# Kernel optimization log

Hardware: AMD Instinct MI355X
Metric: run time of the kernel (lower is better)

Reference implementation:

```python
import jax, jax.numpy as jnp
import numpy as np

MODES = 256


def setup_inputs() -> dict:
    key = jax.random.key(0)
    k1, k2, k3, k4, k5 = jax.random.split(key, 5)
    B, C_IN, C_OUT, N, KM = 8, 128, 128, 8192, 32
    scale = 1.0 / (C_IN * C_OUT)
    return {
        "x": jax.random.normal(k1, (B, C_IN, N), dtype=jnp.float32),
        "wbases": jax.random.normal(k2, (B, N, MODES), dtype=jnp.float32),
        "bases": jax.random.normal(k3, (B, N, MODES), dtype=jnp.float32),
        "weights": scale * jax.random.normal(k4, (C_IN, C_OUT, KM), dtype=jnp.float32),
        "D": jax.random.normal(k5, (KM, MODES), dtype=jnp.float32),
    }


def reference(x, wbases, bases, weights, D):
    # Project onto weighted bases: (b, c_in, n) x (b, n, modes) -> (b, c_in, modes)
    x_hat = jnp.einsum('bcx,bxk->bck', x, wbases[:, :, :MODES])
    # D-weighted channel mixing. Original: x_hat1[b,i,j,k] = x_hat[b,i,k]*D[j,k];
    # y[b,o,k] = sum_{i,j} x_hat1[b,i,j,k] * weights[i,o,j]
    # Equivalent fused contraction (same math, no 4D broadcast):
    y_hat = jnp.einsum('bik,jk,ioj->bok', x_hat, D, weights)
    # Reconstruct on output bases: (b, c_out, modes) x (b, n, modes) -> (b, c_out, n)
    y = jnp.einsum('bck,bxk->bcx', y_hat, bases[:, :, :MODES])
    return y
```

## Files before the change

### kernel.cpp

```cpp
#include <hip/hip_runtime.h>

#define B_    8
#define CIN   128
#define COUT  128
#define NX    8192
#define KMJ   32
#define MODES 256

typedef short bf16x8 __attribute__((ext_vector_type(8)));
typedef float f32x4  __attribute__((ext_vector_type(4)));

__device__ __forceinline__ float bf2f(unsigned short u) {
    union { unsigned int i; float f; } v; v.i = ((unsigned int)u) << 16; return v.f;
}
__device__ __forceinline__ unsigned short f2bf(float f) {
    union { float f; unsigned int i; } v; v.f = f;
    unsigned int x = v.i;
    return (unsigned short)((x + 0x7fffu + ((x >> 16) & 1u)) >> 16);
}
__device__ __forceinline__ bf16x8 cvt8(const float* __restrict__ p) {
    f32x4 a = *(const f32x4*)p;
    f32x4 b = *(const f32x4*)(p + 4);
    bf16x8 r;
    r[0] = (short)f2bf(a[0]); r[1] = (short)f2bf(a[1]);
    r[2] = (short)f2bf(a[2]); r[3] = (short)f2bf(a[3]);
    r[4] = (short)f2bf(b[0]); r[5] = (short)f2bf(b[1]);
    r[6] = (short)f2bf(b[2]); r[7] = (short)f2bf(b[3]);
    return r;
}
__device__ __forceinline__ ushort4 cvt4(f32x4 a) {
    ushort4 r;
    r.x = f2bf(a[0]); r.y = f2bf(a[1]); r.z = f2bf(a[2]); r.w = f2bf(a[3]);
    return r;
}

__global__ __launch_bounds__(256) void k1_wk(const float* __restrict__ W,
                                             const float* __restrict__ D,
                                             unsigned short* __restrict__ Wk) {
    int wave = threadIdx.x >> 6, lane = threadIdx.x & 63;
    int quad = lane >> 4, l16 = lane & 15;
    int gw  = blockIdx.x * 4 + wave;
    int oi0 = gw * 16;
    int i0  = oi0 & 127, o0 = oi0 >> 7;
    bf16x8 bfrag = cvt8(W + ((size_t)(i0 + l16) * COUT + o0) * KMJ + quad * 8);
    for (int mt = 0; mt < 16; mt++) {
        int k0 = mt * 16;
        bf16x8 afrag;
#pragma unroll
        for (int jj = 0; jj < 8; jj++)
            afrag[jj] = (short)f2bf(D[(quad * 8 + jj) * MODES + k0 + l16]);
        f32x4 acc = {0.f, 0.f, 0.f, 0.f};
        acc = __builtin_amdgcn_mfma_f32_16x16x32_bf16(afrag, bfrag, acc, 0, 0, 0);
#pragma unroll
        for (int r = 0; r < 4; r++)
            Wk[(size_t)(k0 + quad * 4 + r) * (CIN * COUT) + oi0 + l16] = f2bf(acc[r]);
    }
}

__global__ __launch_bounds__(512, 4) void k2_xhat(const float* __restrict__ X,
                                                  const float* __restrict__ WB,
                                                  unsigned short* __restrict__ PART) {
    __shared__ __align__(16) unsigned short Xs[128 * 40];
    __shared__ __align__(16) unsigned short WBT[8 * 552];
    int nt = blockIdx.x, b = blockIdx.y, kh = blockIdx.z;
    int r0 = nt * 256;
    int t  = threadIdx.x;
    int wave = t >> 6, lane = t & 63;
    int wm = wave >> 1, wn = wave & 1;
    int quad = lane >> 4, l16 = lane & 15;

    const float* xb  = X  + (size_t)b * CIN * NX;
    const float* wbb = WB + (size_t)b * NX * MODES + kh * 128;

    bool isX = (t >= 256);
    int t2 = t & 255;
    int xn4 = t2 & 7,  xc = t2 >> 3;
    int kq  = t2 & 31, nq = t2 >> 5;

    f32x4 acc[2][4];
#pragma unroll
    for (int i = 0; i < 2; i++)
#pragma unroll
        for (int j = 0; j < 4; j++) acc[i][j] = (f32x4){0.f, 0.f, 0.f, 0.f};

    f32x4 st[4];
    if (isX) {
#pragma unroll
        for (int r = 0; r < 4; r++)
            st[r] = *(const f32x4*)(xb + (size_t)(xc + 32 * r) * NX + r0 + 4 * xn4);
    } else {
#pragma unroll
        for (int r = 0; r < 4; r++)
            st[r] = *(const f32x4*)(wbb + (size_t)(r0 + 4 * nq + r) * MODES + 4 * kq);
    }

    for (int s = 0; s < 8; s++) {
        __syncthreads();
        if (isX) {
#pragma unroll
            for (int r = 0; r < 4; r++)
                *(ushort4*)(Xs + (xc + 32 * r) * 40 + 4 * xn4) = cvt4(st[r]);
        } else {
#pragma unroll
            for (int j = 0; j < 4; j++) {
                int k = 4 * kq + j;
                ushort4 w;
                w.x = f2bf(st[0][j]); w.y = f2bf(st[1][j]);
                w.z = f2bf(st[2][j]); w.w = f2bf(st[3][j]);
                *(ushort4*)(WBT + (k >> 4) * 552 + (k & 15) * 32 + ((k >> 2) & 3) * 8 + 4 * nq) = w;
            }
        }
        __syncthreads();

        if (s < 7) {
            int rs = r0 + (s + 1) * 32;
            if (isX) {
#pragma unroll
                for (int r = 0; r < 4; r++)
                    st[r] = *(const f32x4*)(xb + (size_t)(xc + 32 * r) * NX + rs + 4 * xn4);
            } else {
#pragma unroll
                for (int r = 0; r < 4; r++)
                    st[r] = *(const f32x4*)(wbb + (size_t)(rs + 4 * nq + r) * MODES + 4 * kq);
            }
        }

        bf16x8 af[2], bfv[4];
#pragma unroll
        for (int tm = 0; tm < 2; tm++)
            af[tm] = *(const bf16x8*)(Xs + (wm * 32 + tm * 16 + l16) * 40 + quad * 8);
#pragma unroll
        for (int tn = 0; tn < 4; tn++) {
            int km = wn * 64 + tn * 16 + l16;
            bfv[tn] = *(const bf16x8*)(WBT + (km >> 4) * 552 + (km & 15) * 32 + ((km >> 2) & 3) * 8 + quad * 8);
        }
#pragma unroll
        for (int tm = 0; tm < 2; tm++)
#pragma unroll
            for (int tn = 0; tn < 4; tn++)
                acc[tm][tn] = __builtin_amdgcn_mfma_f32_16x16x32_bf16(af[tm], bfv[tn], acc[tm][tn], 0, 0, 0);
    }

    unsigned short* pb = PART + ((size_t)b * 32 + nt) * (CIN * MODES) + kh * 128;
#pragma unroll
    for (int tm = 0; tm < 2; tm++) {
        int c = wm * 32 + tm * 16 + quad * 4;
#pragma unroll
        for (int tn = 0; tn < 4; tn++) {
            int km = wn * 64 + tn * 16 + l16;
#pragma unroll
            for (int r = 0; r < 4; r++)
                pb[(size_t)(c + r) * MODES + km] = f2bf(acc[tm][tn][r]);
        }
    }
}

__global__ __launch_bounds__(256) void k2b_red(const unsigned short* __restrict__ PART,
                                               float* __restrict__ XH) {
    int e0 = blockIdx.x * 1024 + threadIdx.x;
#pragma unroll
    for (int r = 0; r < 4; r++) {
        int e = e0 + r * 256;
        int b = e >> 15, rem = e & 32767;
        const unsigned short* p = PART + (size_t)b * 32 * (CIN * MODES) + rem;
        float acc = 0.f;
#pragma unroll
        for (int nt = 0; nt < 32; nt++) acc += bf2f(p[nt * (CIN * MODES)]);
        XH[e] = acc;
    }
}

__global__ __launch_bounds__(256) void k3_yhat(const float* __restrict__ XH,
                                               const unsigned short* __restrict__ Wk,
                                               unsigned short* __restrict__ YH) {
    __shared__ float xs[128][8];
    int k = blockIdx.x;
    int t = threadIdx.x;
#pragma unroll
    for (int l = 0; l < 4; l++) {
        int e = l * 256 + t;
        int i = e >> 3, b = e & 7;
        xs[i][b] = XH[(size_t)b * (CIN * MODES) + (size_t)i * MODES + k];
    }
    __syncthreads();
    int o = t & 127, bh = t >> 7;
    const unsigned short* wp = Wk + (size_t)k * (CIN * COUT) + (size_t)o * CIN;
    f32x4 acc = {0.f, 0.f, 0.f, 0.f};
    for (int ii = 0; ii < 16; ii++) {
        bf16x8 wc = *(const bf16x8*)(wp + ii * 8);
#pragma unroll
        for (int jj = 0; jj < 8; jj++) {
            float w = bf2f((unsigned short)wc[jj]);
            f32x4 xv = *(const f32x4*)&xs[ii * 8 + jj][bh * 4];
            acc += w * xv;
        }
    }
#pragma unroll
    for (int r = 0; r < 4; r++)
        YH[((size_t)(bh * 4 + r) * COUT + o) * MODES + k] = f2bf(acc[r]);
}

__global__ __launch_bounds__(256) void k4_y(const unsigned short* __restrict__ YH,
                                            const float* __restrict__ BA,
                                            float* __restrict__ Y) {
    __shared__ __align__(16) unsigned short As[128 * 32];
    __shared__ __align__(16) unsigned short Bs[128 * 32];
    int b  = blockIdx.y;
    int n0 = blockIdx.x * 128;
    int t  = threadIdx.x;
    int wave = t >> 6, lane = t & 63;
    int wm = wave >> 1, wn = wave & 1;
    int quad = lane >> 4, l16 = lane & 15;

    const unsigned short* yhb = YH + (size_t)b * COUT * MODES;
    const float* bab = BA + (size_t)b * NX * MODES + (size_t)n0 * MODES;

    int E0 = t * 8;
    int row0 = E0 >> 5, kk0 = E0 & 31;
    int row1 = (2048 + E0) >> 5, kk1 = (2048 + E0) & 31;

    f32x4 acc[4][4];
#pragma unroll
    for (int i = 0; i < 4; i++)
#pragma unroll
        for (int j = 0; j < 4; j++) acc[i][j] = (f32x4){0.f, 0.f, 0.f, 0.f};

    bf16x8 av0 = *(const bf16x8*)(yhb + (size_t)row0 * MODES + kk0);
    bf16x8 av1 = *(const bf16x8*)(yhb + (size_t)row1 * MODES + kk1);
    f32x4 bv0a = *(const f32x4*)(bab + (size_t)row0 * MODES + kk0);
    f32x4 bv0b = *(const f32x4*)(bab + (size_t)row0 * MODES + kk0 + 4);
    f32x4 bv1a = *(const f32x4*)(bab + (size_t)row1 * MODES + kk1);
    f32x4 bv1b = *(const f32x4*)(bab + (size_t)row1 * MODES + kk1 + 4);

    for (int step = 0; step < 8; step++) {
        __syncthreads();
        *(bf16x8*)(As + E0)        = av0;
        *(bf16x8*)(As + 2048 + E0) = av1;
        bf16x8 bs0, bs1;
        bs0[0]=(short)f2bf(bv0a[0]); bs0[1]=(short)f2bf(bv0a[1]);
        bs0[2]=(short)f2bf(bv0a[2]); bs0[3]=(short)f2bf(bv0a[3]);
        bs0[4]=(short)f2bf(bv0b[0]); bs0[5]=(short)f2bf(bv0b[1]);
        bs0[6]=(short)f2bf(bv0b[2]); bs0[7]=(short)f2bf(bv0b[3]);
        bs1[0]=(short)f2bf(bv1a[0]); bs1[1]=(short)f2bf(bv1a[1]);
        bs1[2]=(short)f2bf(bv1a[2]); bs1[3]=(short)f2bf(bv1a[3]);
        bs1[4]=(short)f2bf(bv1b[0]); bs1[5]=(short)f2bf(bv1b[1]);
        bs1[6]=(short)f2bf(bv1b[2]); bs1[7]=(short)f2bf(bv1b[3]);
        *(bf16x8*)(Bs + E0)        = bs0;
        *(bf16x8*)(Bs + 2048 + E0) = bs1;
        __syncthreads();

        if (step < 7) {
            int ks = (step + 1) * 32;
            av0  = *(const bf16x8*)(yhb + (size_t)row0 * MODES + ks + kk0);
            av1  = *(const bf16x8*)(yhb + (size_t)row1 * MODES + ks + kk1);
            bv0a = *(const f32x4*)(bab + (size_t)row0 * MODES + ks + kk0);
            bv0b = *(const f32x4*)(bab + (size_t)row0 * MODES + ks + kk0 + 4);
            bv1a = *(const f32x4*)(bab + (size_t)row1 * MODES + ks + kk1);
            bv1b = *(const f32x4*)(bab + (size_t)row1 * MODES + ks + kk1 + 4);
        }

        bf16x8 af[4], bfv[4];
#pragma unroll
        for (int tm = 0; tm < 4; tm++) {
            int c = wm * 64 + tm * 16 + l16;
            af[tm] = *(const bf16x8*)(As + c * 32 + quad * 8);
        }
#pragma unroll
        for (int tn = 0; tn < 4; tn++) {
            int n = wn * 64 + tn * 16 + l16;
            bfv[tn] = *(const bf16x8*)(Bs + n * 32 + quad * 8);
        }
#pragma unroll
        for (int tm = 0; tm < 4; tm++)
#pragma unroll
            for (int tn = 0; tn < 4; tn++)
                acc[tm][tn] = __builtin_amdgcn_mfma_f32_16x16x32_bf16(af[tm], bfv[tn], acc[tm][tn], 0, 0, 0);
    }

    float* yb = Y + (size_t)b * COUT * NX;
#pragma unroll
    for (int tm = 0; tm < 4; tm++) {
        int o = wm * 64 + tm * 16 + quad * 4;
#pragma unroll
        for (int tn = 0; tn < 4; tn++) {
            int n = n0 + wn * 64 + tn * 16 + l16;
#pragma unroll
            for (int r = 0; r < 4; r++)
                yb[(size_t)(o + r) * NX + n] = acc[tm][tn][r];
        }
    }
}

extern "C" void kernel_launch(void* const* d_in, const int* in_sizes, int n_in,
                              void* d_out, int out_size, void* d_ws, size_t ws_size,
                              hipStream_t stream) {
    const float* X  = (const float*)d_in[0];
    const float* WB = (const float*)d_in[1];
    const float* BA = (const float*)d_in[2];
    const float* W  = (const float*)d_in[3];
    const float* D  = (const float*)d_in[4];
    float* Y = (float*)d_out;

    char* ws = (char*)d_ws;
    unsigned short* Wk   = (unsigned short*)ws;
    float*          XH   = (float*)(ws + (8u << 20));
    unsigned short* YH   = (unsigned short*)(ws + (9u << 20));
    unsigned short* PART = (unsigned short*)(ws + (10u << 20));

    k1_wk  <<<256,            256, 0, stream>>>(W, D, Wk);
    k2_xhat<<<dim3(32, 8, 2), 512, 0, stream>>>(X, WB, PART);
    k2b_red<<<256,            256, 0, stream>>>(PART, XH);
    k3_yhat<<<MODES,          256, 0, stream>>>(XH, Wk, YH);
    k4_y   <<<dim3(64, 8),    256, 0, stream>>>(YH, BA, Y);
}
```

Measured before the change: 220.4 us.

## Use larger K-chunks and 8-wave tiling in xhat and y GEMM kernels

```diff
diff --git a/kernel.cpp b/kernel.cpp
--- a/kernel.cpp
+++ b/kernel.cpp
@@ -60,94 +60,104 @@
 __global__ __launch_bounds__(512, 4) void k2_xhat(const float* __restrict__ X,
                                                   const float* __restrict__ WB,
                                                   unsigned short* __restrict__ PART) {
-    __shared__ __align__(16) unsigned short Xs[128 * 40];
-    __shared__ __align__(16) unsigned short WBT[8 * 552];
+    __shared__ __align__(16) unsigned short Xs[128 * 72];
+    __shared__ __align__(16) unsigned short WBT[128 * 72];
     int nt = blockIdx.x, b = blockIdx.y, kh = blockIdx.z;
     int r0 = nt * 256;
     int t  = threadIdx.x;
     int wave = t >> 6, lane = t & 63;
-    int wm = wave >> 1, wn = wave & 1;
+    int wm = wave >> 2, wk = wave & 3;
     int quad = lane >> 4, l16 = lane & 15;
 
     const float* xb  = X  + (size_t)b * CIN * NX;
     const float* wbb = WB + (size_t)b * NX * MODES + kh * 128;
 
     bool isX = (t >= 256);
-    int t2 = t & 255;
-    int xn4 = t2 & 7,  xc = t2 >> 3;
-    int kq  = t2 & 31, nq = t2 >> 5;
-
-    f32x4 acc[2][4];
-#pragma unroll
-    for (int i = 0; i < 2; i++)
-#pragma unroll
-        for (int j = 0; j < 4; j++) acc[i][j] = (f32x4){0.f, 0.f, 0.f, 0.f};
-
-    f32x4 st[4];
-    if (isX) {
-#pragma unroll
-        for (int r = 0; r < 4; r++)
-            st[r] = *(const f32x4*)(xb + (size_t)(xc + 32 * r) * NX + r0 + 4 * xn4);
-    } else {
-#pragma unroll
-        for (int r = 0; r < 4; r++)
-            st[r] = *(const f32x4*)(wbb + (size_t)(r0 + 4 * nq + r) * MODES + 4 * kq);
-    }
-
-    for (int s = 0; s < 8; s++) {
+    int j  = t & 255;
+    int xc = j & 127, xh = j >> 7;
+    int kq = j & 31,  ng = j >> 5;
+
+    f32x4 acc[4][2];
+#pragma unroll
+    for (int i = 0; i < 4; i++)
+#pragma unroll
+        for (int jj = 0; jj < 2; jj++) acc[i][jj] = (f32x4){0.f, 0.f, 0.f, 0.f};
+
+    f32x4 st[8];
+
+    {
+        int rs = r0;
+        if (isX) {
+#pragma unroll
+            for (int q = 0; q < 8; q++)
+                st[q] = *(const f32x4*)(xb + (size_t)xc * NX + rs + xh * 32 + 4 * q);
+        } else {
+#pragma unroll
+            for (int g = 0; g < 2; g++)
+#pragma unroll
+                for (int r = 0; r < 4; r++)
+                    st[g * 4 + r] = *(const f32x4*)(wbb + (size_t)(rs + g * 32 + ng * 4 + r) * MODES + 4 * kq);
+        }
+    }
+
+    for (int p = 0; p < 4; p++) {
+        if (p) __syncthreads();
+        if (isX) {
+#pragma unroll
+            for (int q = 0; q < 8; q++)
+                *(ushort4*)(Xs + (size_t)xc * 72 + xh * 32 + 4 * q) = cvt4(st[q]);
+        } else {
+#pragma unroll
+            for (int g = 0; g < 2; g++)
+#pragma unroll
+                for (int j2 = 0; j2 < 4; j2++) {
+                    ushort4 w;
+                    w.x = f2bf(st[g * 4 + 0][j2]); w.y = f2bf(st[g * 4 + 1][j2]);
+                    w.z = f2bf(st[g * 4 + 2][j2]); w.w = f2bf(st[g * 4 + 3][j2]);
+                    *(ushort4*)(WBT + (size_t)(4 * kq + j2) * 72 + g * 32 + ng * 4) = w;
+                }
+        }
         __syncthreads();
-        if (isX) {
-#pragma unroll
-            for (int r = 0; r < 4; r++)
-                *(ushort4*)(Xs + (xc + 32 * r) * 40 + 4 * xn4) = cvt4(st[r]);
-        } else {
-#pragma unroll
-            for (int j = 0; j < 4; j++) {
-                int k = 4 * kq + j;
-                ushort4 w;
-                w.x = f2bf(st[0][j]); w.y = f2bf(st[1][j]);
-                w.z = f2bf(st[2][j]); w.w = f2bf(st[3][j]);
-                *(ushort4*)(WBT + (k >> 4) * 552 + (k & 15) * 32 + ((k >> 2) & 3) * 8 + 4 * nq) = w;
+
+        if (p < 3) {
+            int rs = r0 + (p + 1) * 64;
+            if (isX) {
+#pragma unroll
+                for (int q = 0; q < 8; q++)
+                    st[q] = *(const f32x4*)(xb + (size_t)xc * NX + rs + xh * 32 + 4 * q);
+            } else {
+#pragma unroll
+                for (int g = 0; g < 2; g++)
+#pragma unroll
+                    for (int r = 0; r < 4; r++)
+                        st[g * 4 + r] = *(const f32x4*)(wbb + (size_t)(rs + g * 32 + ng * 4 + r) * MODES + 4 * kq);
             }
         }
-        __syncthreads();
-
-        if (s < 7) {
-            int rs = r0 + (s + 1) * 32;
-            if (isX) {
-#pragma unroll
-                for (int r = 0; r < 4; r++)
-                    st[r] = *(const f32x4*)(xb + (size_t)(xc + 32 * r) * NX + rs + 4 * xn4);
-            } else {
-#pragma unroll
-                for (int r = 0; r < 4; r++)
-                    st[r] = *(const f32x4*)(wbb + (size_t)(rs + 4 * nq + r) * MODES + 4 * kq);
-            }
-        }
-
-        bf16x8 af[2], bfv[4];
-#pragma unroll
-        for (int tm = 0; tm < 2; tm++)
-            af[tm] = *(const bf16x8*)(Xs + (wm * 32 + tm * 16 + l16) * 40 + quad * 8);
-#pragma unroll
-        for (int tn = 0; tn < 4; tn++) {
-            int km = wn * 64 + tn * 16 + l16;
-            bfv[tn] = *(const bf16x8*)(WBT + (km >> 4) * 552 + (km & 15) * 32 + ((km >> 2) & 3) * 8 + quad * 8);
-        }
-#pragma unroll
-        for (int tm = 0; tm < 2; tm++)
-#pragma unroll
-            for (int tn = 0; tn < 4; tn++)
-                acc[tm][tn] = __builtin_amdgcn_mfma_f32_16x16x32_bf16(af[tm], bfv[tn], acc[tm][tn], 0, 0, 0);
+
+#pragma unroll
+        for (int ks = 0; ks < 2; ks++) {
+            bf16x8 af[4], bfv[2];
+#pragma unroll
+            for (int tm = 0; tm < 4; tm++)
+                af[tm] = *(const bf16x8*)(Xs + (size_t)(wm * 64 + tm * 16 + l16) * 72 + ks * 32 + quad * 8);
+#pragma unroll
+            for (int tn = 0; tn < 2; tn++)
+                bfv[tn] = *(const bf16x8*)(WBT + (size_t)(wk * 32 + tn * 16 + l16) * 72 + ks * 32 + quad * 8);
+#pragma unroll
+            for (int tm = 0; tm < 4; tm++)
+#pragma unroll
+                for (int tn = 0; tn < 2; tn++)
+                    acc[tm][tn] = __builtin_amdgcn_mfma_f32_16x16x32_bf16(af[tm], bfv[tn], acc[tm][tn], 0, 0, 0);
+        }
     }
 
     unsigned short* pb = PART + ((size_t)b * 32 + nt) * (CIN * MODES) + kh * 128;
 #pragma unroll
-    for (int tm = 0; tm < 2; tm++) {
-        int c = wm * 32 + tm * 16 + quad * 4;
-#pragma unroll
-        for (int tn = 0; tn < 4; tn++) {
-            int km = wn * 64 + tn * 16 + l16;
+    for (int tm = 0; tm < 4; tm++) {
+        int c = wm * 64 + tm * 16 + quad * 4;
+#pragma unroll
+        for (int tn = 0; tn < 2; tn++) {
+            int km = wk * 32 + tn * 16 + l16;
 #pragma unroll
             for (int r = 0; r < 4; r++)
                 pb[(size_t)(c + r) * MODES + km] = f2bf(acc[tm][tn][r]);
@@ -200,81 +210,73 @@
         YH[((size_t)(bh * 4 + r) * COUT + o) * MODES + k] = f2bf(acc[r]);
 }
 
-__global__ __launch_bounds__(256) void k4_y(const unsigned short* __restrict__ YH,
-                                            const float* __restrict__ BA,
-                                            float* __restrict__ Y) {
-    __shared__ __align__(16) unsigned short As[128 * 32];
-    __shared__ __align__(16) unsigned short Bs[128 * 32];
+__global__ __launch_bounds__(512, 4) void k4_y(const unsigned short* __restrict__ YH,
+                                               const float* __restrict__ BA,
+                                               float* __restrict__ Y) {
+    __shared__ __align__(16) unsigned short As[128 * 136];
+    __shared__ __align__(16) unsigned short Bs[128 * 136];
     int b  = blockIdx.y;
     int n0 = blockIdx.x * 128;
     int t  = threadIdx.x;
     int wave = t >> 6, lane = t & 63;
-    int wm = wave >> 1, wn = wave & 1;
+    int wm = wave >> 2, wn2 = wave & 3;
     int quad = lane >> 4, l16 = lane & 15;
 
     const unsigned short* yhb = YH + (size_t)b * COUT * MODES;
     const float* bab = BA + (size_t)b * NX * MODES + (size_t)n0 * MODES;
 
-    int E0 = t * 8;
-    int row0 = E0 >> 5, kk0 = E0 & 31;
-    int row1 = (2048 + E0) >> 5, kk1 = (2048 + E0) & 31;
-
-    f32x4 acc[4][4];
+    int rc = t & 127, rq = t >> 7;
+
+    f32x4 acc[4][2];
 #pragma unroll
     for (int i = 0; i < 4; i++)
 #pragma unroll
-        for (int j = 0; j < 4; j++) acc[i][j] = (f32x4){0.f, 0.f, 0.f, 0.f};
-
-    bf16x8 av0 = *(const bf16x8*)(yhb + (size_t)row0 * MODES + kk0);
-    bf16x8 av1 = *(const bf16x8*)(yhb + (size_t)row1 * MODES + kk1);
-    f32x4 bv0a = *(const f32x4*)(bab + (size_t)row0 * MODES + kk0);
-    f32x4 bv0b = *(const f32x4*)(bab + (size_t)row0 * MODES + kk0 + 4);
-    f32x4 bv1a = *(const f32x4*)(bab + (size_t)row1 * MODES + kk1);
-    f32x4 bv1b = *(const f32x4*)(bab + (size_t)row1 * MODES + kk1 + 4);
-
-    for (int step = 0; step < 8; step++) {
+        for (int jj = 0; jj < 2; jj++) acc[i][jj] = (f32x4){0.f, 0.f, 0.f, 0.f};
+
+    bf16x8 av[4];
+    f32x4  bv[8];
+
+#pragma unroll
+    for (int q = 0; q < 4; q++)
+        av[q] = *(const bf16x8*)(yhb + (size_t)rc * MODES + rq * 32 + 8 * q);
+#pragma unroll
+    for (int q = 0; q < 8; q++)
+        bv[q] = *(const f32x4*)(bab + (size_t)rc * MODES + rq * 32 + 4 * q);
+
+    for (int p = 0; p < 2; p++) {
+        if (p) __syncthreads();
+#pragma unroll
+        for (int q = 0; q < 4; q++)
+            *(bf16x8*)(As + (size_t)rc * 136 + rq * 32 + 8 * q) = av[q];
+#pragma unroll
+        for (int q = 0; q < 8; q++)
+            *(ushort4*)(Bs + (size_t)rc * 136 + rq * 32 + 4 * q) = cvt4(bv[q]);
         __syncthreads();
-        *(bf16x8*)(As + E0)        = av0;
-        *(bf16x8*)(As + 2048 + E0) = av1;
-        bf16x8 bs0, bs1;
-        bs0[0]=(short)f2bf(bv0a[0]); bs0[1]=(short)f2bf(bv0a[1]);
-        bs0[2]=(short)f2bf(bv0a[2]); bs0[3]=(short)f2bf(bv0a[3]);
-        bs0[4]=(short)f2bf(bv0b[0]); bs0[5]=(short)f2bf(bv0b[1]);
-        bs0[6]=(short)f2bf(bv0b[2]); bs0[7]=(short)f2bf(bv0b[3]);
-        bs1[0]=(short)f2bf(bv1a[0]); bs1[1]=(short)f2bf(bv1a[1]);
-        bs1[2]=(short)f2bf(bv1a[2]); bs1[3]=(short)f2bf(bv1a[3]);
-        bs1[4]=(short)f2bf(bv1b[0]); bs1[5]=(short)f2bf(bv1b[1]);
-        bs1[6]=(short)f2bf(bv1b[2]); bs1[7]=(short)f2bf(bv1b[3]);
-        *(bf16x8*)(Bs + E0)        = bs0;
-        *(bf16x8*)(Bs + 2048 + E0) = bs1;
-        __syncthreads();
-
-        if (step < 7) {
-            int ks = (step + 1) * 32;
-            av0  = *(const bf16x8*)(yhb + (size_t)row0 * MODES + ks + kk0);
-            av1  = *(const bf16x8*)(yhb + (size_t)row1 * MODES + ks + kk1);
-            bv0a = *(const f32x4*)(bab + (size_t)row0 * MODES + ks + kk0);
-            bv0b = *(const f32x4*)(bab + (size_t)row0 * MODES + ks + kk0 + 4);
-            bv1a = *(const f32x4*)(bab + (size_t)row1 * MODES + ks + kk1);
-            bv1b = *(const f32x4*)(bab + (size_t)row1 * MODES + ks + kk1 + 4);
-        }
-
-        bf16x8 af[4], bfv[4];
-#pragma unroll
-        for (int tm = 0; tm < 4; tm++) {
-            int c = wm * 64 + tm * 16 + l16;
-            af[tm] = *(const bf16x8*)(As + c * 32 + quad * 8);
-        }
-#pragma unroll
-        for (int tn = 0; tn < 4; tn++) {
-            int n = wn * 64 + tn * 16 + l16;
-            bfv[tn] = *(const bf16x8*)(Bs + n * 32 + quad * 8);
-        }
-#pragma unroll
-        for (int tm = 0; tm < 4; tm++)
-#pragma unroll
-            for (int tn = 0; tn < 4; tn++)
-                acc[tm][tn] = __builtin_amdgcn_mfma_f32_16x16x32_bf16(af[tm], bfv[tn], acc[tm][tn], 0, 0, 0);
+
+        if (p == 0) {
+#pragma unroll
+            for (int q = 0; q < 4; q++)
+                av[q] = *(const bf16x8*)(yhb + (size_t)rc * MODES + 128 + rq * 32 + 8 * q);
+#pragma unroll
+            for (int q = 0; q < 8; q++)
+                bv[q] = *(const f32x4*)(bab + (size_t)rc * MODES + 128 + rq * 32 + 4 * q);
+        }
+
+#pragma unroll
+        for (int ks = 0; ks < 4; ks++) {
+            bf16x8 af[4], bfv[2];
+#pragma unroll
+            for (int tm = 0; tm < 4; tm++)
+                af[tm] = *(const bf16x8*)(As + (size_t)(wm * 64 + tm * 16 + l16) * 136 + ks * 32 + quad * 8);
+#pragma unroll
+            for (int tn = 0; tn < 2; tn++)
+                bfv[tn] = *(const bf16x8*)(Bs + (size_t)(wn2 * 32 + tn * 16 + l16) * 136 + ks * 32 + quad * 8);
+#pragma unroll
+            for (int tm = 0; tm < 4; tm++)
+#pragma unroll
+                for (int tn = 0; tn < 2; tn++)
+                    acc[tm][tn] = __builtin_amdgcn_mfma_f32_16x16x32_bf16(af[tm], bfv[tn], acc[tm][tn], 0, 0, 0);
+        }
     }
 
     float* yb = Y + (size_t)b * COUT * NX;
@@ -282,8 +284,8 @@
     for (int tm = 0; tm < 4; tm++) {
         int o = wm * 64 + tm * 16 + quad * 4;
 #pragma unroll
-        for (int tn = 0; tn < 4; tn++) {
-            int n = n0 + wn * 64 + tn * 16 + l16;
+        for (int tn = 0; tn < 2; tn++) {
+            int n = n0 + wn2 * 32 + tn * 16 + l16;
 #pragma unroll
             for (int r = 0; r < 4; r++)
                 yb[(size_t)(o + r) * NX + n] = acc[tm][tn][r];
@@ -311,5 +313,5 @@
     k2_xhat<<<dim3(32, 8, 2), 512, 0, stream>>>(X, WB, PART);
     k2b_red<<<256,            256, 0, stream>>>(PART, XH);
     k3_yhat<<<MODES,          256, 0, stream>>>(XH, Wk, YH);
-    k4_y   <<<dim3(64, 8),    256, 0, stream>>>(YH, BA, Y);
-}
+    k4_y   <<<dim3(64, 8),    512, 0, stream>>>(YH, BA, Y);
+}
```

New measurement: 224.7 us. Within noise of the previous version (+2.0%).
